# Kernel tuning notes

Hardware: AMD Instinct MI355X
Metric: run time of the kernel (lower is better)

## Reference

```python
import jax, jax.numpy as jnp
import numpy as np

B, S, D, E = 2, 2048, 1024, 16  # batch, cutoff (seq), dmodel, n_experts


def setup_inputs() -> dict:
    key = jax.random.key(0)
    k = jax.random.split(key, 6)
    scale = 1.0 / np.sqrt(D)
    return {
        "x": jax.random.normal(k[0], (B, S, D), dtype=jnp.float32),
        "gate": jax.random.normal(k[1], (D, E), dtype=jnp.float32) * scale,
        "W1": jax.random.normal(k[2], (E, D, D), dtype=jnp.float32) * scale,  # lin1: Linear(dmodel, dmodel*E), split per expert
        "b1": jnp.zeros((E, D), dtype=jnp.float32),
        "W2": jax.random.normal(k[3], (E, D, D), dtype=jnp.float32) * scale,  # lin2: Linear(dmodel*E, dmodel), split per expert
        "b2": jnp.zeros((D,), dtype=jnp.float32),
        "topk": 256,
    }


def reference(x, gate, W1, b1, W2, b2, topk):
    # Expert-choice gating: softmax over the token (cutoff) axis per expert.
    logits = jnp.einsum("bsd,de->bse", x, gate)            # (B, S, E)
    probs = jax.nn.softmax(logits, axis=1)                  # softmax over tokens
    # Each expert selects its top-k tokens.
    g, idx = jax.lax.top_k(jnp.swapaxes(probs, 1, 2), topk)  # (B, E, k)
    # Gather selected tokens: (B, E, k, D)
    xin = jnp.take_along_axis(x[:, None, :, :], idx[..., None], axis=2)
    # Per-expert 2-layer FFN (hidden size = dmodel, per width = dmodel*n_experts)
    h = jax.nn.relu(jnp.einsum("bekd,edf->bekf", xin, W1) + b1[None, :, None, :])
    out = jnp.einsum("bekf,efd->bekd", h, W2) + b2           # (B, E, k, D)
    weighted = out * g[..., None]
    # Scatter-add back to token positions.
    y = jnp.zeros_like(x)
    b_idx = jnp.arange(x.shape[0])[:, None, None]            # (B, 1, 1)
    y = y.at[b_idx, idx].add(weighted)
    return y
```

## Files before the change

### kernel.cpp

```cpp
#include <hip/hip_runtime.h>
#include <stdint.h>
#include <math.h>

constexpr int CB = 2;
constexpr int CS = 2048;
constexpr int CD = 1024;
constexpr int CE = 16;
constexpr int CK = 256;

typedef short bf16x8 __attribute__((ext_vector_type(8)));
typedef float f32x4 __attribute__((ext_vector_type(4)));

typedef __attribute__((address_space(1))) const unsigned int gu32;
typedef __attribute__((address_space(3))) unsigned int lu32;
typedef __attribute__((address_space(3))) unsigned short lds_us;

__device__ __forceinline__ void async16(const void* g, lds_us* l) {
    __builtin_amdgcn_global_load_lds((gu32*)g, (lu32*)l, 16, 0, 0);
}

__device__ __forceinline__ bf16x8 ds_read128(const lds_us* p) {
    bf16x8 v;
    asm volatile("ds_read_b128 %0, %1" : "=v"(v) : "v"(p));
    return v;
}

__device__ inline unsigned short f2bf(float f) {
    union { float f; uint32_t u; } v; v.f = f;
    uint32_t u = v.u;
    uint32_t r = (u + 0x7FFFu + ((u >> 16) & 1u)) >> 16;
    return (unsigned short)r;
}

__global__ __launch_bounds__(256)
void logits_part_kernel(const float* __restrict__ x,
                        const float* __restrict__ gate,
                        float* __restrict__ part) {
    const int tt = blockIdx.x;
    const int dt = blockIdx.y;
    const int tid = threadIdx.x;

    __shared__ float Xs[256 * 17];

    float acc[CE];
#pragma unroll
    for (int e = 0; e < CE; e++) acc[e] = 0.0f;

    const int tokl = tid >> 2;
    const int c4 = (tid & 3) << 2;

    for (int dch = 0; dch < 4; dch++) {
        const int dbase = dt * 64 + dch * 16;
        __syncthreads();
#pragma unroll
        for (int q = 0; q < 4; q++) {
            const int tok = q * 64 + tokl;
            const f32x4 v = *(const f32x4*)(x + ((size_t)(tt * 256 + tok)) * CD + dbase + c4);
            Xs[tok * 17 + c4 + 0] = v[0];
            Xs[tok * 17 + c4 + 1] = v[1];
            Xs[tok * 17 + c4 + 2] = v[2];
            Xs[tok * 17 + c4 + 3] = v[3];
        }
        __syncthreads();
#pragma unroll
        for (int d = 0; d < 16; d++) {
            const float xv = Xs[tid * 17 + d];
            const float* gr = gate + (size_t)(dbase + d) * CE;
#pragma unroll
            for (int e = 0; e < CE; e++) acc[e] = fmaf(xv, gr[e], acc[e]);
        }
    }
    float* pr = part + ((size_t)dt * (CB * CS) + tt * 256 + tid) * CE;
#pragma unroll
    for (int e = 0; e < CE; e++) pr[e] = acc[e];
}

__global__ __launch_bounds__(256)
void logits_reduce_kernel(const float* __restrict__ part,
                          float* __restrict__ logits) {
    const int i = blockIdx.x * 256 + threadIdx.x;
    float s = 0.0f;
#pragma unroll
    for (int p = 0; p < 16; p++) s += part[(size_t)p * (CB * CS * CE) + i];
    logits[i] = s;
}

__global__ void topk_kernel(const float* __restrict__ logits,
                            int* __restrict__ idx_out,
                            float* __restrict__ g_out) {
    const int be = blockIdx.x;
    const int b = be >> 4, e = be & 15;
    const int tid = threadIdx.x;
    const int lane = tid & 63, wid = tid >> 6;

    __shared__ float redf[4];
    __shared__ int hist[256];
    __shared__ int wsum[4];
    __shared__ int sh_bin, sh_rank;
    __shared__ int scnt, eqc;
    __shared__ int eqbuf[CS];

    float lv[8], p[8];
    unsigned int uv[8];
#pragma unroll
    for (int j = 0; j < 8; j++) {
        const int s = tid + j * 256;
        lv[j] = logits[((size_t)(b * CS + s)) * CE + e];
    }
    float m = lv[0];
#pragma unroll
    for (int j = 1; j < 8; j++) m = fmaxf(m, lv[j]);
#pragma unroll
    for (int o = 32; o > 0; o >>= 1) m = fmaxf(m, __shfl_down(m, o));
    if (lane == 0) redf[wid] = m;
    __syncthreads();
    m = fmaxf(fmaxf(redf[0], redf[1]), fmaxf(redf[2], redf[3]));
    __syncthreads();
    float lsum = 0.0f;
#pragma unroll
    for (int j = 0; j < 8; j++) {
        p[j] = expf(lv[j] - m);
        uv[j] = __float_as_uint(p[j]);
        lsum += p[j];
    }
#pragma unroll
    for (int o = 32; o > 0; o >>= 1) lsum += __shfl_down(lsum, o);
    if (lane == 0) redf[wid] = lsum;
    __syncthreads();
    const float total = redf[0] + redf[1] + redf[2] + redf[3];
    const float inv_total = 1.0f / total;

    unsigned int prefix = 0;
    int kneed = CK;
    for (int pass = 0; pass < 4; pass++) {
        const int shift = 24 - 8 * pass;
        __syncthreads();
        hist[tid] = 0;
        __syncthreads();
        const unsigned int hmask = (pass == 0) ? 0u : (0xFFFFFFFFu << (shift + 8));
#pragma unroll
        for (int j = 0; j < 8; j++)
            if ((uv[j] & hmask) == prefix)
                atomicAdd(&hist[(uv[j] >> shift) & 255], 1);
        __syncthreads();
        const int own = hist[tid];
        int s = own;
#pragma unroll
        for (int o = 1; o < 64; o <<= 1) {
            int t = __shfl_down(s, o);
            if (lane + o < 64) s += t;
        }
        if (lane == 0) wsum[wid] = s;
        __syncthreads();
        int above = 0;
        for (int ww = wid + 1; ww < 4; ww++) above += wsum[ww];
        const int incl = s + above;
        if (incl >= kneed && (incl - own) < kneed) {
            sh_bin = tid;
            sh_rank = kneed - (incl - own);
        }
        __syncthreads();
        prefix |= ((unsigned int)sh_bin) << shift;
        kneed = sh_rank;
    }
    const unsigned int v = prefix;
    const int quota = kneed;

    if (tid == 0) { scnt = 0; eqc = 0; }
    __syncthreads();
#pragma unroll
    for (int j = 0; j < 8; j++) {
        const int s = tid + j * 256;
        if (uv[j] > v) {
            const int pos = atomicAdd(&scnt, 1);
            idx_out[be * CK + pos] = s;
            g_out[be * CK + pos] = p[j] * inv_total;
        } else if (uv[j] == v) {
            const int pos = atomicAdd(&eqc, 1);
            eqbuf[pos] = s;
        }
    }
    __syncthreads();
    if (tid == 0) {
        const int cgt = scnt;
        const int n = eqc;
        const float gv = __uint_as_float(v) * inv_total;
        if (n > quota) {
            for (int i = 0; i < quota; i++) {
                int mn = i;
                for (int k2 = i + 1; k2 < n; k2++)
                    if (eqbuf[k2] < eqbuf[mn]) mn = k2;
                const int t2 = eqbuf[i]; eqbuf[i] = eqbuf[mn]; eqbuf[mn] = t2;
            }
        }
        for (int i = 0; i < quota; i++) {
            idx_out[be * CK + cgt + i] = eqbuf[i];
            g_out[be * CK + cgt + i] = gv;
        }
    }
}

__global__ void gather_kernel(const float* __restrict__ x,
                              const int* __restrict__ idx_ws,
                              unsigned short* __restrict__ xinbuf) {
    const int row = blockIdx.x;
    const int be = row >> 8;
    const int b = be >> 4;
    const int tok = idx_ws[row];
    const int c0 = threadIdx.x * 4;
    const f32x4 f = *(const f32x4*)(x + ((size_t)b * CS + tok) * CD + c0);
    union { unsigned short u[4]; uint2 v; } t;
    t.u[0] = f2bf(f[0]); t.u[1] = f2bf(f[1]); t.u[2] = f2bf(f[2]); t.u[3] = f2bf(f[3]);
    *(uint2*)(xinbuf + (size_t)row * CD + c0) = t.v;
}

__global__ __launch_bounds__(256)
void wt_kernel(const float* __restrict__ W, unsigned short* __restrict__ Wt) {
    const int kt = blockIdx.x, nt = blockIdx.y, e = blockIdx.z;
    const float* src = W + (size_t)e * CD * CD;
    unsigned short* dst = Wt + (size_t)e * CD * CD;
    const int tid = threadIdx.x;
    __shared__ unsigned short T[64 * 64];

    const int kr = tid >> 4;
    const int n4 = (tid & 15) << 2;
#pragma unroll
    for (int it = 0; it < 4; it++) {
        const int k = it * 16 + kr;
        const f32x4 v = *(const f32x4*)(src + (size_t)(kt * 64 + k) * CD + nt * 64 + n4);
        const int pp = k >> 4;
        const int klo = k & 15;
#pragma unroll
        for (int i = 0; i < 4; i++) {
            const int n = n4 + i;
            T[n * 64 + ((pp ^ ((n >> 2) & 3)) << 4) + klo] = f2bf(v[i]);
        }
    }
    __syncthreads();
    const int n = tid >> 2;
    const int pp = tid & 3;
    const int sw = pp ^ ((n >> 2) & 3);
    const uint4 a = *(const uint4*)&T[n * 64 + (sw << 4)];
    const uint4 b = *(const uint4*)&T[n * 64 + (sw << 4) + 8];
    unsigned short* drow = dst + (size_t)(nt * 64 + n) * CD + kt * 64 + pp * 16;
    *(uint4*)drow = a;
    *(uint4*)(drow + 8) = b;
}

#define MFMA16(A_, B_, C_) __builtin_amdgcn_mfma_f32_16x16x32_bf16((A_), (B_), (C_), 0, 0, 0)

template <int PHASE>
__global__ __launch_bounds__(512, 2)
void ffn_gemm(const unsigned short* __restrict__ Ain,
              const unsigned short* __restrict__ Wt,
              const float* __restrict__ bias,
              unsigned short* __restrict__ hout,
              const int* __restrict__ idx_ws,
              const float* __restrict__ g_ws,
              float* __restrict__ y) {
    const int id = blockIdx.x;
    const int xcd = id & 7;
    const int q = id >> 3;
    const int e = ((q & 1) << 3) | xcd;
    const int b = (q >> 1) & 1;
    const int ntile = q >> 2;
    const int be = b * CE + e;
    const int tid = threadIdx.x;
    const int w = tid >> 6, l = tid & 63;
    const int wm = w >> 1, wn = w & 1;
    const int quad = l >> 4, lr = l & 15;

    __shared__ __align__(16) unsigned short LA[3][256 * 64];
    __shared__ __align__(16) unsigned short LB[3][128 * 64];

    f32x4 acc[4][4];
    const f32x4 zz = {0.f, 0.f, 0.f, 0.f};
#pragma unroll
    for (int mi = 0; mi < 4; mi++)
#pragma unroll
        for (int ni = 0; ni < 4; ni++) acc[mi][ni] = zz;

    const unsigned short* Agb = Ain + (size_t)be * CK * CD;
    const unsigned short* Bgb = Wt + ((size_t)e * CD + ntile * 128) * CD;

    const unsigned short* pAg[4]; int dA[4];
#pragma unroll
    for (int j = 0; j < 4; j++) {
        const int u = w * 256 + j * 64 + l;
        const int row = u >> 3;
        const int c = (u & 7) ^ (row & 7);
        pAg[j] = Agb + (size_t)row * CD + c * 8;
        dA[j] = u * 8;
    }
    const unsigned short* pBg[2]; int dB[2];
#pragma unroll
    for (int j = 0; j < 2; j++) {
        const int u = w * 128 + j * 64 + l;
        const int row = u >> 3;
        const int c = (u & 7) ^ (row & 7);
        pBg[j] = Bgb + (size_t)row * CD + c * 8;
        dB[j] = u * 8;
    }

    const int sc0 = (quad ^ (lr & 7)) * 8;
    const int sc1 = ((quad ^ (lr & 7)) ^ 4) * 8;
    int offA[2][4], offB[2][4];
#pragma unroll
    for (int mi = 0; mi < 4; mi++) {
        const int r = wm * 64 + mi * 16 + lr;
        offA[0][mi] = r * 64 + sc0;
        offA[1][mi] = r * 64 + sc1;
    }
#pragma unroll
    for (int ni = 0; ni < 4; ni++) {
        const int r = wn * 64 + ni * 16 + lr;
        offB[0][ni] = r * 64 + sc0;
        offB[1][ni] = r * 64 + sc1;
    }

    lds_us* pA0 = (lds_us*)LA[0]; lds_us* pA1 = (lds_us*)LA[1]; lds_us* pA2 = (lds_us*)LA[2];
    lds_us* pB0 = (lds_us*)LB[0]; lds_us* pB1 = (lds_us*)LB[1]; lds_us* pB2 = (lds_us*)LB[2];

#pragma unroll
    for (int j = 0; j < 4; j++) async16(pAg[j], pA0 + dA[j]);
#pragma unroll
    for (int j = 0; j < 2; j++) async16(pBg[j], pB0 + dB[j]);
#pragma unroll
    for (int j = 0; j < 4; j++) async16(pAg[j] + 64, pA1 + dA[j]);
#pragma unroll
    for (int j = 0; j < 2; j++) async16(pBg[j] + 64, pB1 + dB[j]);
    asm volatile("s_waitcnt vmcnt(6)" ::: "memory");
    asm volatile("s_barrier" ::: "memory");

    for (int t = 0; t < 16; t++) {
        const bool pf = (t + 2) < 16;
        const int kel = (t + 2) * 64;
        bf16x8 a0, a1, a2, a3, b0, b1, b2, b3;

        a0 = ds_read128(pA0 + offA[0][0]);
        a1 = ds_read128(pA0 + offA[0][1]);
        a2 = ds_read128(pA0 + offA[0][2]);
        a3 = ds_read128(pA0 + offA[0][3]);
        b0 = ds_read128(pB0 + offB[0][0]);
        b1 = ds_read128(pB0 + offB[0][1]);
        if (pf) { async16(pAg[0] + kel, pA2 + dA[0]); async16(pAg[1] + kel, pA2 + dA[1]); }
        asm volatile("s_barrier" ::: "memory");
        asm volatile("s_waitcnt lgkmcnt(0)"
                     : "+v"(a0), "+v"(a1), "+v"(a2), "+v"(a3), "+v"(b0), "+v"(b1) :: "memory");
        __builtin_amdgcn_s_setprio(1);
        acc[0][0] = MFMA16(a0, b0, acc[0][0]);
        acc[1][0] = MFMA16(a1, b0, acc[1][0]);
        acc[2][0] = MFMA16(a2, b0, acc[2][0]);
        acc[3][0] = MFMA16(a3, b0, acc[3][0]);
        acc[0][1] = MFMA16(a0, b1, acc[0][1]);
        acc[1][1] = MFMA16(a1, b1, acc[1][1]);
        acc[2][1] = MFMA16(a2, b1, acc[2][1]);
        acc[3][1] = MFMA16(a3, b1, acc[3][1]);
        __builtin_amdgcn_s_setprio(0);
        asm volatile("s_barrier" ::: "memory");

        b2 = ds_read128(pB0 + offB[0][2]);
        b3 = ds_read128(pB0 + offB[0][3]);
        if (pf) { async16(pAg[2] + kel, pA2 + dA[2]); async16(pAg[3] + kel, pA2 + dA[3]); }
        asm volatile("s_barrier" ::: "memory");
        asm volatile("s_waitcnt lgkmcnt(0)" : "+v"(b2), "+v"(b3) :: "memory");
        __builtin_amdgcn_s_setprio(1);
        acc[0][2] = MFMA16(a0, b2, acc[0][2]);
        acc[1][2] = MFMA16(a1, b2, acc[1][2]);
        acc[2][2] = MFMA16(a2, b2, acc[2][2]);
        acc[3][2] = MFMA16(a3, b2, acc[3][2]);
        acc[0][3] = MFMA16(a0, b3, acc[0][3]);
        acc[1][3] = MFMA16(a1, b3, acc[1][3]);
        acc[2][3] = MFMA16(a2, b3, acc[2][3]);
        acc[3][3] = MFMA16(a3, b3, acc[3][3]);
        __builtin_amdgcn_s_setprio(0);
        asm volatile("s_barrier" ::: "memory");

        a0 = ds_read128(pA0 + offA[1][0]);
        a1 = ds_read128(pA0 + offA[1][1]);
        a2 = ds_read128(pA0 + offA[1][2]);
        a3 = ds_read128(pA0 + offA[1][3]);
        b0 = ds_read128(pB0 + offB[1][0]);
        b1 = ds_read128(pB0 + offB[1][1]);
        if (pf) { async16(pBg[0] + kel, pB2 + dB[0]); async16(pBg[1] + kel, pB2 + dB[1]); }
        asm volatile("s_barrier" ::: "memory");
        asm volatile("s_waitcnt lgkmcnt(0)"
                     : "+v"(a0), "+v"(a1), "+v"(a2), "+v"(a3), "+v"(b0), "+v"(b1) :: "memory");
        __builtin_amdgcn_s_setprio(1);
        acc[0][0] = MFMA16(a0, b0, acc[0][0]);
        acc[1][0] = MFMA16(a1, b0, acc[1][0]);
        acc[2][0] = MFMA16(a2, b0, acc[2][0]);
        acc[3][0] = MFMA16(a3, b0, acc[3][0]);
        acc[0][1] = MFMA16(a0, b1, acc[0][1]);
        acc[1][1] = MFMA16(a1, b1, acc[1][1]);
        acc[2][1] = MFMA16(a2, b1, acc[2][1]);
        acc[3][1] = MFMA16(a3, b1, acc[3][1]);
        __builtin_amdgcn_s_setprio(0);
        asm volatile("s_barrier" ::: "memory");

        b2 = ds_read128(pB0 + offB[1][2]);
        b3 = ds_read128(pB0 + offB[1][3]);
        asm volatile("s_barrier" ::: "memory");
        asm volatile("s_waitcnt lgkmcnt(0)" : "+v"(b2), "+v"(b3) :: "memory");
        __builtin_amdgcn_s_setprio(1);
        acc[0][2] = MFMA16(a0, b2, acc[0][2]);
        acc[1][2] = MFMA16(a1, b2, acc[1][2]);
        acc[2][2] = MFMA16(a2, b2, acc[2][2]);
        acc[3][2] = MFMA16(a3, b2, acc[3][2]);
        acc[0][3] = MFMA16(a0, b3, acc[0][3]);
        acc[1][3] = MFMA16(a1, b3, acc[1][3]);
        acc[2][3] = MFMA16(a2, b3, acc[2][3]);
        acc[3][3] = MFMA16(a3, b3, acc[3][3]);
        __builtin_amdgcn_s_setprio(0);
        if (t < 14)       asm volatile("s_waitcnt vmcnt(6)" ::: "memory");
        else if (t == 14) asm volatile("s_waitcnt vmcnt(0)" ::: "memory");
        asm volatile("s_barrier" ::: "memory");

        lds_us* tp = pA0; pA0 = pA1; pA1 = pA2; pA2 = tp;
        tp = pB0; pB0 = pB1; pB1 = pB2; pB2 = tp;
    }

    const int gn_base = ntile * 128 + wn * 64;
    if (PHASE == 0) {
#pragma unroll
        for (int mi = 0; mi < 4; mi++)
#pragma unroll
            for (int r = 0; r < 4; r++) {
                const int slot = wm * 64 + mi * 16 + quad * 4 + r;
                unsigned short* outrow = hout + ((size_t)be * CK + slot) * CD;
#pragma unroll
                for (int ni = 0; ni < 4; ni++) {
                    const int col = gn_base + ni * 16 + lr;
                    float hv = acc[mi][ni][r] + bias[e * CD + col];
                    hv = fmaxf(hv, 0.0f);
                    outrow[col] = f2bf(hv);
                }
            }
    } else {
#pragma unroll
        for (int mi = 0; mi < 4; mi++)
#pragma unroll
            for (int r = 0; r < 4; r++) {
                const int slot = wm * 64 + mi * 16 + quad * 4 + r;
                const int tok = idx_ws[be * CK + slot];
                const float gval = g_ws[be * CK + slot];
                float* yrow = y + ((size_t)b * CS + tok) * CD;
#pragma unroll
                for (int ni = 0; ni < 4; ni++) {
                    const int col = gn_base + ni * 16 + lr;
                    const float val = (acc[mi][ni][r] + bias[col]) * gval;
                    atomicAdd(&yrow[col], val);
                }
            }
    }
}

extern "C" void kernel_launch(void* const* d_in, const int* in_sizes, int n_in,
                              void* d_out, int out_size, void* d_ws, size_t ws_size,
                              hipStream_t stream) {
    const float* x    = (const float*)d_in[0];
    const float* gate = (const float*)d_in[1];
    const float* W1   = (const float*)d_in[2];
    const float* b1   = (const float*)d_in[3];
    const float* W2   = (const float*)d_in[4];
    const float* b2   = (const float*)d_in[5];
    float* y = (float*)d_out;

    char* ws = (char*)d_ws;
    float* logits = (float*)ws;
    int* idxw = (int*)(ws + 262144);
    float* gw = (float*)(ws + 294912);
    unsigned short* xinbuf = (unsigned short*)(ws + 327680);
    unsigned short* hbuf = (unsigned short*)(ws + 17104896);
    float* partbuf = (float*)(ws + 17104896);
    unsigned short* wtbuf = (unsigned short*)(ws + 33882112);

    logits_part_kernel<<<dim3(16, 16), 256, 0, stream>>>(x, gate, partbuf);
    logits_reduce_kernel<<<CB * CS * CE / 256, 256, 0, stream>>>(partbuf, logits);
    topk_kernel<<<CB * CE, 256, 0, stream>>>(logits, idxw, gw);
    gather_kernel<<<CB * CE * CK, 256, 0, stream>>>(x, idxw, xinbuf);
    wt_kernel<<<dim3(16, 16, CE), 256, 0, stream>>>(W1, wtbuf);
    hipMemsetAsync(d_out, 0, (size_t)CB * CS * CD * sizeof(float), stream);
    ffn_gemm<0><<<256, 512, 0, stream>>>(xinbuf, wtbuf, b1, hbuf, idxw, gw, y);
    wt_kernel<<<dim3(16, 16, CE), 256, 0, stream>>>(W2, wtbuf);
    ffn_gemm<1><<<256, 512, 0, stream>>>(hbuf, wtbuf, b2, nullptr, idxw, gw, y);
}
```

Measured before the change: 282.0 us.

## Fuse gather with W1 transpose, fold y zeroing into logits, merge GEMM barrier phases

Zeroing of y moves into the logits partial kernel, replacing the separate memset. The gather and the W1 transpose/convert now run as one combined prep launch, saving a kernel launch and letting the two tasks overlap. Inside the GEMM main loop, all four B fragments are read from LDS up front, which cuts the barrier count per k-step in half and reorders the async prefetches. Launch bounds drop from 2 to 1 block per CU, giving more registers at the cost of occupancy.

```diff
diff --git a/kernel.cpp b/kernel.cpp
--- a/kernel.cpp
+++ b/kernel.cpp
@@ -35,10 +35,19 @@
 __global__ __launch_bounds__(256)
 void logits_part_kernel(const float* __restrict__ x,
                         const float* __restrict__ gate,
-                        float* __restrict__ part) {
+                        float* __restrict__ part,
+                        float* __restrict__ y) {
     const int tt = blockIdx.x;
     const int dt = blockIdx.y;
     const int tid = threadIdx.x;
+
+    {
+        const int bb = dt * 16 + tt;
+        float* yb = y + (size_t)bb * 16384 + tid * 4;
+        const f32x4 z = {0.f, 0.f, 0.f, 0.f};
+#pragma unroll
+        for (int i = 0; i < 16; i++) *(f32x4*)(yb + i * 1024) = z;
+    }
 
     __shared__ float Xs[256 * 17];
 
@@ -200,27 +209,11 @@
     }
 }
 
-__global__ void gather_kernel(const float* __restrict__ x,
-                              const int* __restrict__ idx_ws,
-                              unsigned short* __restrict__ xinbuf) {
-    const int row = blockIdx.x;
-    const int be = row >> 8;
-    const int b = be >> 4;
-    const int tok = idx_ws[row];
-    const int c0 = threadIdx.x * 4;
-    const f32x4 f = *(const f32x4*)(x + ((size_t)b * CS + tok) * CD + c0);
-    union { unsigned short u[4]; uint2 v; } t;
-    t.u[0] = f2bf(f[0]); t.u[1] = f2bf(f[1]); t.u[2] = f2bf(f[2]); t.u[3] = f2bf(f[3]);
-    *(uint2*)(xinbuf + (size_t)row * CD + c0) = t.v;
-}
-
-__global__ __launch_bounds__(256)
-void wt_kernel(const float* __restrict__ W, unsigned short* __restrict__ Wt) {
-    const int kt = blockIdx.x, nt = blockIdx.y, e = blockIdx.z;
+__device__ __forceinline__
+void wt_body(const float* __restrict__ W, unsigned short* __restrict__ Wt,
+             int kt, int nt, int e, int tid, unsigned short* T) {
     const float* src = W + (size_t)e * CD * CD;
     unsigned short* dst = Wt + (size_t)e * CD * CD;
-    const int tid = threadIdx.x;
-    __shared__ unsigned short T[64 * 64];
 
     const int kr = tid >> 4;
     const int n4 = (tid & 15) << 2;
@@ -247,10 +240,37 @@
     *(uint4*)(drow + 8) = b;
 }
 
+__global__ __launch_bounds__(256)
+void wt_kernel(const float* __restrict__ W, unsigned short* __restrict__ Wt) {
+    __shared__ unsigned short T[64 * 64];
+    wt_body(W, Wt, blockIdx.x, blockIdx.y, blockIdx.z, threadIdx.x, T);
+}
+
+__global__ __launch_bounds__(256)
+void prep_kernel(const float* __restrict__ W1, unsigned short* __restrict__ Wt,
+                 const float* __restrict__ x, const int* __restrict__ idx_ws,
+                 unsigned short* __restrict__ xinbuf) {
+    __shared__ unsigned short T[64 * 64];
+    const int bx = blockIdx.x;
+    if (bx < 4096) {
+        wt_body(W1, Wt, bx & 15, (bx >> 4) & 15, bx >> 8, threadIdx.x, T);
+    } else {
+        const int row = bx - 4096;
+        const int be = row >> 8;
+        const int b = be >> 4;
+        const int tok = idx_ws[row];
+        const int c0 = threadIdx.x * 4;
+        const f32x4 f = *(const f32x4*)(x + ((size_t)b * CS + tok) * CD + c0);
+        union { unsigned short u[4]; uint2 v; } t;
+        t.u[0] = f2bf(f[0]); t.u[1] = f2bf(f[1]); t.u[2] = f2bf(f[2]); t.u[3] = f2bf(f[3]);
+        *(uint2*)(xinbuf + (size_t)row * CD + c0) = t.v;
+    }
+}
+
 #define MFMA16(A_, B_, C_) __builtin_amdgcn_mfma_f32_16x16x32_bf16((A_), (B_), (C_), 0, 0, 0)
 
 template <int PHASE>
-__global__ __launch_bounds__(512, 2)
+__global__ __launch_bounds__(512, 1)
 void ffn_gemm(const unsigned short* __restrict__ Ain,
               const unsigned short* __restrict__ Wt,
               const float* __restrict__ bias,
@@ -343,10 +363,17 @@
         a3 = ds_read128(pA0 + offA[0][3]);
         b0 = ds_read128(pB0 + offB[0][0]);
         b1 = ds_read128(pB0 + offB[0][1]);
-        if (pf) { async16(pAg[0] + kel, pA2 + dA[0]); async16(pAg[1] + kel, pA2 + dA[1]); }
+        b2 = ds_read128(pB0 + offB[0][2]);
+        b3 = ds_read128(pB0 + offB[0][3]);
+        if (pf) {
+            async16(pAg[0] + kel, pA2 + dA[0]);
+            async16(pAg[1] + kel, pA2 + dA[1]);
+            async16(pAg[2] + kel, pA2 + dA[2]);
+        }
         asm volatile("s_barrier" ::: "memory");
         asm volatile("s_waitcnt lgkmcnt(0)"
-                     : "+v"(a0), "+v"(a1), "+v"(a2), "+v"(a3), "+v"(b0), "+v"(b1) :: "memory");
+                     : "+v"(a0), "+v"(a1), "+v"(a2), "+v"(a3),
+                       "+v"(b0), "+v"(b1), "+v"(b2), "+v"(b3) :: "memory");
         __builtin_amdgcn_s_setprio(1);
         acc[0][0] = MFMA16(a0, b0, acc[0][0]);
         acc[1][0] = MFMA16(a1, b0, acc[1][0]);
@@ -356,15 +383,6 @@
         acc[1][1] = MFMA16(a1, b1, acc[1][1]);
         acc[2][1] = MFMA16(a2, b1, acc[2][1]);
         acc[3][1] = MFMA16(a3, b1, acc[3][1]);
-        __builtin_amdgcn_s_setprio(0);
-        asm volatile("s_barrier" ::: "memory");
-
-        b2 = ds_read128(pB0 + offB[0][2]);
-        b3 = ds_read128(pB0 + offB[0][3]);
-        if (pf) { async16(pAg[2] + kel, pA2 + dA[2]); async16(pAg[3] + kel, pA2 + dA[3]); }
-        asm volatile("s_barrier" ::: "memory");
-        asm volatile("s_waitcnt lgkmcnt(0)" : "+v"(b2), "+v"(b3) :: "memory");
-        __builtin_amdgcn_s_setprio(1);
         acc[0][2] = MFMA16(a0, b2, acc[0][2]);
         acc[1][2] = MFMA16(a1, b2, acc[1][2]);
         acc[2][2] = MFMA16(a2, b2, acc[2][2]);
@@ -382,10 +400,17 @@
         a3 = ds_read128(pA0 + offA[1][3]);
         b0 = ds_read128(pB0 + offB[1][0]);
         b1 = ds_read128(pB0 + offB[1][1]);
-        if (pf) { async16(pBg[0] + kel, pB2 + dB[0]); async16(pBg[1] + kel, pB2 + dB[1]); }
+        b2 = ds_read128(pB0 + offB[1][2]);
+        b3 = ds_read128(pB0 + offB[1][3]);
+        if (pf) {
+            async16(pAg[3] + kel, pA2 + dA[3]);
+            async16(pBg[0] + kel, pB2 + dB[0]);
+            async16(pBg[1] + kel, pB2 + dB[1]);
+        }
         asm volatile("s_barrier" ::: "memory");
         asm volatile("s_waitcnt lgkmcnt(0)"
-                     : "+v"(a0), "+v"(a1), "+v"(a2), "+v"(a3), "+v"(b0), "+v"(b1) :: "memory");
+                     : "+v"(a0), "+v"(a1), "+v"(a2), "+v"(a3),
+                       "+v"(b0), "+v"(b1), "+v"(b2), "+v"(b3) :: "memory");
         __builtin_amdgcn_s_setprio(1);
         acc[0][0] = MFMA16(a0, b0, acc[0][0]);
         acc[1][0] = MFMA16(a1, b0, acc[1][0]);
@@ -395,14 +420,6 @@
         acc[1][1] = MFMA16(a1, b1, acc[1][1]);
         acc[2][1] = MFMA16(a2, b1, acc[2][1]);
         acc[3][1] = MFMA16(a3, b1, acc[3][1]);
-        __builtin_amdgcn_s_setprio(0);
-        asm volatile("s_barrier" ::: "memory");
-
-        b2 = ds_read128(pB0 + offB[1][2]);
-        b3 = ds_read128(pB0 + offB[1][3]);
-        asm volatile("s_barrier" ::: "memory");
-        asm volatile("s_waitcnt lgkmcnt(0)" : "+v"(b2), "+v"(b3) :: "memory");
-        __builtin_amdgcn_s_setprio(1);
         acc[0][2] = MFMA16(a0, b2, acc[0][2]);
         acc[1][2] = MFMA16(a1, b2, acc[1][2]);
         acc[2][2] = MFMA16(a2, b2, acc[2][2]);
@@ -475,12 +492,10 @@
     float* partbuf = (float*)(ws + 17104896);
     unsigned short* wtbuf = (unsigned short*)(ws + 33882112);
 
-    logits_part_kernel<<<dim3(16, 16), 256, 0, stream>>>(x, gate, partbuf);
+    logits_part_kernel<<<dim3(16, 16), 256, 0, stream>>>(x, gate, partbuf, y);
     logits_reduce_kernel<<<CB * CS * CE / 256, 256, 0, stream>>>(partbuf, logits);
     topk_kernel<<<CB * CE, 256, 0, stream>>>(logits, idxw, gw);
-    gather_kernel<<<CB * CE * CK, 256, 0, stream>>>(x, idxw, xinbuf);
-    wt_kernel<<<dim3(16, 16, CE), 256, 0, stream>>>(W1, wtbuf);
-    hipMemsetAsync(d_out, 0, (size_t)CB * CS * CD * sizeof(float), stream);
+    prep_kernel<<<4096 + CB * CE * CK, 256, 0, stream>>>(W1, wtbuf, x, idxw, xinbuf);
     ffn_gemm<0><<<256, 512, 0, stream>>>(xinbuf, wtbuf, b1, hbuf, idxw, gw, y);
     wt_kernel<<<dim3(16, 16, CE), 256, 0, stream>>>(W2, wtbuf);
     ffn_gemm<1><<<256, 512, 0, stream>>>(hbuf, wtbuf, b2, nullptr, idxw, gw, y);
```

Result: faster. 271.8 us (-3.6%).
